# Optimization experiments

Hardware: AMD Instinct MI355X
Metric: run time of the kernel (lower is better)

Reference implementation:

```python
import jax, jax.numpy as jnp
import numpy as np

NB_CLASSES = 256
EMBEDDING_SIZE = 50
TOTAL_CHARS = 8_000_000
NUM_WORDS = 1_600_000


def setup_inputs() -> dict:
    key = jax.random.key(0)
    k1, k2, k3 = jax.random.split(key, 3)
    char_ids = jax.random.randint(k1, (TOTAL_CHARS,), 0, NB_CLASSES, dtype=jnp.int64 if jax.config.jax_enable_x64 else jnp.int32)
    segment_ids = jnp.sort(jax.random.randint(k2, (TOTAL_CHARS,), 0, NUM_WORDS, dtype=char_ids.dtype))
    embedding_table = jax.random.normal(k3, (NB_CLASSES, EMBEDDING_SIZE), dtype=jnp.float32)
    return {
        "char_ids": char_ids,
        "segment_ids": segment_ids,
        "num_words": NUM_WORDS,
        "embedding_table": embedding_table,
    }


def reference(char_ids, segment_ids, num_words, embedding_table):
    # Fused ragged gather + segment-mean: equivalent to, for each word,
    # mean over its characters of embedding_table[char].
    char_emb = embedding_table[char_ids]                      # [total_chars, E]
    sums = jax.ops.segment_sum(char_emb, segment_ids, num_segments=num_words)  # [num_words, E]
    counts = jax.ops.segment_sum(
        jnp.ones((char_ids.shape[0],), dtype=embedding_table.dtype),
        segment_ids, num_segments=num_words)                  # [num_words]
    counts = jnp.maximum(counts, 1.0)                         # guard empty words
    return sums / counts[:, None]                             # [num_words, E]
```

## Files before the change

kernel.cpp:

```cpp
#include <hip/hip_runtime.h>


#define NB 256
#define EMB 50
#define PAIRS 25
#define BLK 1024

__global__ __launch_bounds__(256) void seg_starts4(
    const int* __restrict__ seg, int* __restrict__ starts, int n, int nw) {
  int base = (blockIdx.x * blockDim.x + threadIdx.x) * 4;
  if (base >= n) return;
  int lim = n - base; if (lim > 4) lim = 4;
  int vals[4];
  if (lim == 4) {
    int4 v = *(const int4*)(seg + base);
    vals[0] = v.x; vals[1] = v.y; vals[2] = v.z; vals[3] = v.w;
  } else {
    for (int u = 0; u < lim; ++u) vals[u] = seg[base + u];
  }
  int prev = (base > 0) ? seg[base - 1] : -1;
  for (int u = 0; u < lim; ++u) {
    int cur = vals[u];
    for (int w = prev + 1; w <= cur; ++w) starts[w] = base + u;
    prev = cur;
  }
  if (base + lim == n) {
    for (int w = prev + 1; w <= nw; ++w) starts[w] = n;
  }
}

__global__ __launch_bounds__(BLK, 8) void word_mean_v2(
    const int* __restrict__ char_ids, const float* __restrict__ table,
    const int* __restrict__ starts, float2* __restrict__ out2, int num_words) {
  __shared__ __align__(16) float tab[NB * EMB];
  for (int idx = threadIdx.x; idx < NB * EMB / 4; idx += BLK)
    ((float4*)tab)[idx] = ((const float4*)table)[idx];
  __syncthreads();

  const int total  = num_words * PAIRS;
  const int stride = gridDim.x * BLK;
  for (int t = blockIdx.x * BLK + threadIdx.x; t < total; t += stride) {
    int w  = t / PAIRS;
    int k2 = (t - w * PAIRS) * 2;
    int s = starts[w];
    int e = starts[w + 1];
    float sx = 0.f, sy = 0.f;
    for (int i = s; i < e; ++i) {
      int c = char_ids[i];
      float2 v = *(const float2*)(tab + c * EMB + k2);
      sx += v.x; sy += v.y;
    }
    int cnt = e - s;
    float inv = (cnt > 0) ? (1.0f / (float)cnt) : 0.0f;
    out2[t] = make_float2(sx * inv, sy * inv);
  }
}

__device__ __forceinline__ int lb(const int* __restrict__ seg, int n, int w) {
  int lo = 0, hi = n;
  while (lo < hi) { int m = (lo + hi) >> 1; if (seg[m] < w) lo = m + 1; else hi = m; }
  return lo;
}
__global__ __launch_bounds__(256) void word_mean_bs_kernel(
    const int* __restrict__ char_ids, const int* __restrict__ seg,
    const float* __restrict__ table, float* __restrict__ out, int n, int num_words) {
  int w = blockIdx.x * blockDim.x + threadIdx.x;
  if (w >= num_words) return;
  int s = lb(seg, n, w), e = lb(seg, n, w + 1);
  float ax[PAIRS], ay[PAIRS];
#pragma unroll
  for (int k = 0; k < PAIRS; ++k) { ax[k] = 0.f; ay[k] = 0.f; }
  for (int i = s; i < e; ++i) {
    const float2* row = (const float2*)(table + char_ids[i] * EMB);
#pragma unroll
    for (int k = 0; k < PAIRS; ++k) { float2 v = row[k]; ax[k] += v.x; ay[k] += v.y; }
  }
  int cnt = e - s;
  float inv = (cnt > 0) ? (1.0f / (float)cnt) : 0.0f;
  float2* orow = (float2*)(out + (size_t)w * EMB);
#pragma unroll
  for (int k = 0; k < PAIRS; ++k) orow[k] = make_float2(ax[k] * inv, ay[k] * inv);
}

extern "C" void kernel_launch(void* const* d_in, const int* in_sizes, int n_in,
                              void* d_out, int out_size, void* d_ws, size_t ws_size,
                              hipStream_t stream) {
  const int*   char_ids = (const int*)d_in[0];
  const int*   seg      = (const int*)d_in[1];
  const float* table    = (const float*)d_in[3];
  float*       out      = (float*)d_out;

  const int n  = in_sizes[0];
  const int nw = out_size / EMB;

  if (ws_size >= (size_t)(nw + 1) * sizeof(int)) {
    int* starts = (int*)d_ws;
    int nchunk = (n + 3) / 4;
    seg_starts4<<<(nchunk + 255) / 256, 256, 0, stream>>>(seg, starts, n, nw);
    word_mean_v2<<<512, BLK, 0, stream>>>(char_ids, table, starts,
                                          (float2*)out, nw);
  } else {
    word_mean_bs_kernel<<<(nw + 255) / 256, 256, 0, stream>>>(
        char_ids, seg, table, out, n, nw);
  }
}
```

Before: 546.9 us.

## Assign one word per 32-lane group and unroll char-id loads

Restructures the word-mean kernel so each group of 32 threads owns one word, with 25 active lanes each handling one float2 column pair. This replaces the per-thread divide/modulo mapping, and all lanes in a group now read the same starts and char_ids entries, which should broadcast. The character loop is unrolled by 8 with predicated loads to expose memory-level parallelism. In exchange, 7 of every 32 lanes sit idle, wasting about 22% of thread slots. The launch-bounds occupancy hint is also dropped.

```diff
diff --git a/kernel.cpp b/kernel.cpp
--- a/kernel.cpp
+++ b/kernel.cpp
@@ -5,6 +5,7 @@
 #define EMB 50
 #define PAIRS 25
 #define BLK 1024
+#define UNROLL 8
 
 __global__ __launch_bounds__(256) void seg_starts4(
     const int* __restrict__ seg, int* __restrict__ starts, int n, int nw) {
@@ -29,7 +30,7 @@
   }
 }
 
-__global__ __launch_bounds__(BLK, 8) void word_mean_v2(
+__global__ __launch_bounds__(BLK) void word_mean_v3(
     const int* __restrict__ char_ids, const float* __restrict__ table,
     const int* __restrict__ starts, float2* __restrict__ out2, int num_words) {
   __shared__ __align__(16) float tab[NB * EMB];
@@ -37,22 +38,39 @@
     ((float4*)tab)[idx] = ((const float4*)table)[idx];
   __syncthreads();
 
-  const int total  = num_words * PAIRS;
-  const int stride = gridDim.x * BLK;
-  for (int t = blockIdx.x * BLK + threadIdx.x; t < total; t += stride) {
-    int w  = t / PAIRS;
-    int k2 = (t - w * PAIRS) * 2;
+  const int k      = threadIdx.x & 31;
+  const int g      = threadIdx.x >> 5;
+  const bool active = (k < PAIRS);
+  const int k2     = (active ? k : 0) * 2;
+  const int wstep  = gridDim.x * (BLK / 32);
+
+  for (int w = blockIdx.x * (BLK / 32) + g; w < num_words; w += wstep) {
     int s = starts[w];
     int e = starts[w + 1];
+    int cnt = e - s;
+    if (!active) e = s;
     float sx = 0.f, sy = 0.f;
-    for (int i = s; i < e; ++i) {
-      int c = char_ids[i];
-      float2 v = *(const float2*)(tab + c * EMB + k2);
-      sx += v.x; sy += v.y;
+
+    for (int i = s; i < e; i += UNROLL) {
+      int cs[UNROLL];
+#pragma unroll
+      for (int j = 0; j < UNROLL; ++j) {
+        int idx = i + j;
+        cs[j] = (idx < e) ? char_ids[idx] : -1;
+      }
+#pragma unroll
+      for (int j = 0; j < UNROLL; ++j) {
+        if (cs[j] >= 0) {
+          float2 v = *(const float2*)(tab + cs[j] * EMB + k2);
+          sx += v.x; sy += v.y;
+        }
+      }
     }
-    int cnt = e - s;
-    float inv = (cnt > 0) ? (1.0f / (float)cnt) : 0.0f;
-    out2[t] = make_float2(sx * inv, sy * inv);
+
+    if (active) {
+      float inv = (cnt > 0) ? (1.0f / (float)cnt) : 0.0f;
+      out2[(size_t)w * PAIRS + k] = make_float2(sx * inv, sy * inv);
+    }
   }
 }
 
@@ -69,17 +87,17 @@
   int s = lb(seg, n, w), e = lb(seg, n, w + 1);
   float ax[PAIRS], ay[PAIRS];
 #pragma unroll
-  for (int k = 0; k < PAIRS; ++k) { ax[k] = 0.f; ay[k] = 0.f; }
+  for (int p = 0; p < PAIRS; ++p) { ax[p] = 0.f; ay[p] = 0.f; }
   for (int i = s; i < e; ++i) {
     const float2* row = (const float2*)(table + char_ids[i] * EMB);
 #pragma unroll
-    for (int k = 0; k < PAIRS; ++k) { float2 v = row[k]; ax[k] += v.x; ay[k] += v.y; }
+    for (int p = 0; p < PAIRS; ++p) { float2 v = row[p]; ax[p] += v.x; ay[p] += v.y; }
   }
   int cnt = e - s;
   float inv = (cnt > 0) ? (1.0f / (float)cnt) : 0.0f;
   float2* orow = (float2*)(out + (size_t)w * EMB);
 #pragma unroll
-  for (int k = 0; k < PAIRS; ++k) orow[k] = make_float2(ax[k] * inv, ay[k] * inv);
+  for (int p = 0; p < PAIRS; ++p) orow[p] = make_float2(ax[p] * inv, ay[p] * inv);
 }
 
 extern "C" void kernel_launch(void* const* d_in, const int* in_sizes, int n_in,
@@ -97,7 +115,7 @@
     int* starts = (int*)d_ws;
     int nchunk = (n + 3) / 4;
     seg_starts4<<<(nchunk + 255) / 256, 256, 0, stream>>>(seg, starts, n, nw);
-    word_mean_v2<<<512, BLK, 0, stream>>>(char_ids, table, starts,
+    word_mean_v3<<<512, BLK, 0, stream>>>(char_ids, table, starts,
                                           (float2*)out, nw);
   } else {
     word_mean_bs_kernel<<<(nw + 255) / 256, 256, 0, stream>>>(
```

New measurement: 498.5 us. 8.9% less time.

## Map one wavefront per word with scalar char loads and lane-per-dim accumulation

Applied to the files above, without the earlier changes.

Replaces the thread-per-(word, pair) mapping with one 64-lane wavefront per word, where each lane accumulates one embedding dimension. Word bounds and character ids are made wave-uniform via readfirstlane, so they can be fetched once per wave as scalar loads instead of being loaded redundantly by every thread. The character loop is unrolled by 8 and 4 to expose more independent loads. This wastes 14 of 64 lanes, and whether the scalar loads become faster memory access is not guaranteed.

```diff
diff --git a/kernel.cpp b/kernel.cpp
--- a/kernel.cpp
+++ b/kernel.cpp
@@ -3,8 +3,8 @@
 
 #define NB 256
 #define EMB 50
-#define PAIRS 25
 #define BLK 1024
+#define WPB (BLK / 64)
 
 __global__ __launch_bounds__(256) void seg_starts4(
     const int* __restrict__ seg, int* __restrict__ starts, int n, int nw) {
@@ -29,30 +29,52 @@
   }
 }
 
-__global__ __launch_bounds__(BLK, 8) void word_mean_v2(
+#define RFL(x) __builtin_amdgcn_readfirstlane(x)
+
+__global__ __launch_bounds__(BLK) void word_mean_v4(
     const int* __restrict__ char_ids, const float* __restrict__ table,
-    const int* __restrict__ starts, float2* __restrict__ out2, int num_words) {
+    const int* __restrict__ starts, float* __restrict__ out, int num_words) {
   __shared__ __align__(16) float tab[NB * EMB];
   for (int idx = threadIdx.x; idx < NB * EMB / 4; idx += BLK)
     ((float4*)tab)[idx] = ((const float4*)table)[idx];
   __syncthreads();
 
-  const int total  = num_words * PAIRS;
-  const int stride = gridDim.x * BLK;
-  for (int t = blockIdx.x * BLK + threadIdx.x; t < total; t += stride) {
-    int w  = t / PAIRS;
-    int k2 = (t - w * PAIRS) * 2;
-    int s = starts[w];
-    int e = starts[w + 1];
-    float sx = 0.f, sy = 0.f;
-    for (int i = s; i < e; ++i) {
-      int c = char_ids[i];
-      float2 v = *(const float2*)(tab + c * EMB + k2);
-      sx += v.x; sy += v.y;
+  const int lane = threadIdx.x & 63;
+  const int k    = (lane < EMB) ? lane : (EMB - 1);
+  const int wid0 = RFL(blockIdx.x * WPB + (threadIdx.x >> 6));
+  const int nwv  = gridDim.x * WPB;
+
+  for (int w = wid0; w < num_words; w += nwv) {
+    const int s = RFL(starts[w]);
+    const int e = RFL(starts[w + 1]);
+    float acc = 0.f;
+    int i = s;
+
+    for (; i + 8 <= e; i += 8) {
+      int c0 = RFL(char_ids[i + 0]); int c1 = RFL(char_ids[i + 1]);
+      int c2 = RFL(char_ids[i + 2]); int c3 = RFL(char_ids[i + 3]);
+      int c4 = RFL(char_ids[i + 4]); int c5 = RFL(char_ids[i + 5]);
+      int c6 = RFL(char_ids[i + 6]); int c7 = RFL(char_ids[i + 7]);
+      acc += tab[c0 * EMB + k]; acc += tab[c1 * EMB + k];
+      acc += tab[c2 * EMB + k]; acc += tab[c3 * EMB + k];
+      acc += tab[c4 * EMB + k]; acc += tab[c5 * EMB + k];
+      acc += tab[c6 * EMB + k]; acc += tab[c7 * EMB + k];
     }
-    int cnt = e - s;
-    float inv = (cnt > 0) ? (1.0f / (float)cnt) : 0.0f;
-    out2[t] = make_float2(sx * inv, sy * inv);
+    if (i + 4 <= e) {
+      int c0 = RFL(char_ids[i + 0]); int c1 = RFL(char_ids[i + 1]);
+      int c2 = RFL(char_ids[i + 2]); int c3 = RFL(char_ids[i + 3]);
+      acc += tab[c0 * EMB + k]; acc += tab[c1 * EMB + k];
+      acc += tab[c2 * EMB + k]; acc += tab[c3 * EMB + k];
+      i += 4;
+    }
+    for (; i < e; ++i) {
+      int c = RFL(char_ids[i]);
+      acc += tab[c * EMB + k];
+    }
+
+    const int cnt = e - s;
+    const float inv = (cnt > 0) ? (1.0f / (float)cnt) : 0.0f;
+    if (lane < EMB) out[(size_t)w * EMB + lane] = acc * inv;
   }
 }
 
@@ -67,19 +89,19 @@
   int w = blockIdx.x * blockDim.x + threadIdx.x;
   if (w >= num_words) return;
   int s = lb(seg, n, w), e = lb(seg, n, w + 1);
-  float ax[PAIRS], ay[PAIRS];
+  float ax[25], ay[25];
 #pragma unroll
-  for (int k = 0; k < PAIRS; ++k) { ax[k] = 0.f; ay[k] = 0.f; }
+  for (int p = 0; p < 25; ++p) { ax[p] = 0.f; ay[p] = 0.f; }
   for (int i = s; i < e; ++i) {
     const float2* row = (const float2*)(table + char_ids[i] * EMB);
 #pragma unroll
-    for (int k = 0; k < PAIRS; ++k) { float2 v = row[k]; ax[k] += v.x; ay[k] += v.y; }
+    for (int p = 0; p < 25; ++p) { float2 v = row[p]; ax[p] += v.x; ay[p] += v.y; }
   }
   int cnt = e - s;
   float inv = (cnt > 0) ? (1.0f / (float)cnt) : 0.0f;
   float2* orow = (float2*)(out + (size_t)w * EMB);
 #pragma unroll
-  for (int k = 0; k < PAIRS; ++k) orow[k] = make_float2(ax[k] * inv, ay[k] * inv);
+  for (int p = 0; p < 25; ++p) orow[p] = make_float2(ax[p] * inv, ay[p] * inv);
 }
 
 extern "C" void kernel_launch(void* const* d_in, const int* in_sizes, int n_in,
@@ -97,8 +119,7 @@
     int* starts = (int*)d_ws;
     int nchunk = (n + 3) / 4;
     seg_starts4<<<(nchunk + 255) / 256, 256, 0, stream>>>(seg, starts, n, nw);
-    word_mean_v2<<<512, BLK, 0, stream>>>(char_ids, table, starts,
-                                          (float2*)out, nw);
+    word_mean_v4<<<512, BLK, 0, stream>>>(char_ids, table, starts, out, nw);
   } else {
     word_mean_bs_kernel<<<(nw + 255) / 256, 256, 0, stream>>>(
         char_ids, seg, table, out, n, nw);
```

After: 556.4 us. About the same (+1.7%).
